# Optimization experiments

Measured on AMD Instinct MI355X. Metric: run time of the kernel, lower is better.

The kernel has to match this reference:

```python
import jax, jax.numpy as jnp
import numpy as np

N_NODES = 131072
N_EDGES = 2097152
F_IN = 128
G_NODES = 256  # nodes per graph (equal-size graphs -> ptr = arange(0, N+1, 256))


def _linear(x, W, b):
    return x @ W + b


def _gin_conv(x, src, dst, W1, b1, W2, b2):
    # GINConv with eps=0: MLP(x + sum_{j->i} x_j)
    agg = jax.ops.segment_sum(x[src], dst, num_segments=x.shape[0])
    h = jax.nn.relu(_linear(x + agg, W1, b1))
    return _linear(h, W2, b2)


def _init(key, fan_in, fan_out):
    kw, kb = jax.random.split(key)
    s = 1.0 / np.sqrt(fan_in)
    W = jax.random.uniform(kw, (fan_in, fan_out), jnp.float32, -s, s)
    b = jax.random.uniform(kb, (fan_out,), jnp.float32, -s, s)
    return W, b


def setup_inputs() -> dict:
    key = jax.random.key(0)
    ks = jax.random.split(key, 14)
    x = jax.random.normal(ks[0], (N_NODES, F_IN), jnp.float32)
    edge_index = jax.random.randint(ks[1], (2, N_EDGES), 0, N_NODES, jnp.int64)
    W1a, b1a = _init(ks[2], F_IN, 128)
    W2a, b2a = _init(ks[3], 128, 128)
    W1b, b1b = _init(ks[4], 128, 128)
    W2b, b2b = _init(ks[5], 128, 128)
    Ws1, bs1 = _init(ks[6], 128, 32)
    Ws2, bs2 = _init(ks[7], 32, 32)
    Ws3, bs3 = _init(ks[8], 32, 32)
    Wm1, bm1 = _init(ks[9], 32 * 32, 32)
    Wm2, bm2 = _init(ks[10], 32, 32)
    Wm3, bm3 = _init(ks[11], 32, 2)
    return dict(x=x, edge_index=edge_index,
                W1a=W1a, b1a=b1a, W2a=W2a, b2a=b2a,
                W1b=W1b, b1b=b1b, W2b=W2b, b2b=b2b,
                Ws1=Ws1, bs1=bs1, Ws2=Ws2, bs2=bs2, Ws3=Ws3, bs3=bs3,
                Wm1=Wm1, bm1=bm1, Wm2=Wm2, bm2=bm2, Wm3=Wm3, bm3=bm3,
                nodes_per_graph=G_NODES)


def reference(x, edge_index, W1a, b1a, W2a, b2a, W1b, b1b, W2b, b2b,
              Ws1, bs1, Ws2, bs2, Ws3, bs3,
              Wm1, bm1, Wm2, bm2, Wm3, bm3, nodes_per_graph):
    src, dst = edge_index[0], edge_index[1]
    # two GINConv layers, each followed by outer ReLU (as in forward)
    h = jax.nn.relu(_gin_conv(x, src, dst, W1a, b1a, W2a, b2a))
    h = jax.nn.relu(_gin_conv(h, src, dst, W1b, b1b, W2b, b2b))
    # dropout is identity in eval mode; F.normalize(dim=1) row-wise L2
    hn = h / jnp.maximum(jnp.linalg.norm(h, axis=1, keepdims=True), 1e-12)
    s = jax.nn.relu(_linear(hn, Ws1, bs1))
    s = jax.nn.relu(_linear(s, Ws2, bs2))
    s = jax.nn.relu(_linear(s, Ws3, bs3))  # [N, 32]
    G = x.shape[0] // nodes_per_graph
    sg = s.reshape(G, nodes_per_graph, 32)
    # per-graph second-order pooling: graph.T @ graph, flattened
    HH = jnp.einsum('gnf,gne->gfe', sg, sg).reshape(G, 32 * 32)  # [G, 1024]
    o = jax.nn.relu(_linear(HH, Wm1, bm1))
    o = jax.nn.relu(_linear(o, Wm2, bm2))
    out = jax.nn.relu(_linear(o, Wm3, bm3))  # [G, 2]; output dropout identity in eval
    return (HH, out)
```

## Files before the change

kernel.cpp:

```cpp
#include <hip/hip_runtime.h>
#include <hip/hip_bf16.h>


#define NN 131072
#define NE 2097152
#define NG 512
#define NB 1024
#define ECAP 2560
#define CCAP 3328
#define ECH 8192

typedef unsigned short u16;
typedef unsigned int u32;
typedef __attribute__((ext_vector_type(8))) short short8;
typedef __attribute__((ext_vector_type(4))) float f32x4;

__device__ __forceinline__ float bf2f(u16 u) {
    union { u32 i; float f; } x; x.i = ((u32)u) << 16; return x.f;
}
__device__ __forceinline__ u16 f2bf(float f) {
    union { u32 i; float f; } x; x.f = f;
    u32 r = x.i + 0x7fffu + ((x.i >> 16) & 1u);
    return (u16)(r >> 16);
}

__global__ __launch_bounds__(256) void cast_x(const float* __restrict__ xf,
                                              u16* __restrict__ xb) {
    int i = blockIdx.x * 256 + threadIdx.x;
    const float4* src = (const float4*)xf;
    float4 a = src[2 * i], b = src[2 * i + 1];
    uint4 o;
    o.x = (u32)f2bf(a.x) | ((u32)f2bf(a.y) << 16);
    o.y = (u32)f2bf(a.z) | ((u32)f2bf(a.w) << 16);
    o.z = (u32)f2bf(b.x) | ((u32)f2bf(b.y) << 16);
    o.w = (u32)f2bf(b.z) | ((u32)f2bf(b.w) << 16);
    ((uint4*)xb)[i] = o;
}

__global__ __launch_bounds__(128) void zero_tail(u16* __restrict__ X0,
                                                 u16* __restrict__ H1) {
    int t = threadIdx.x;
    u32* a = (u32*)(X0 + (size_t)NN * 128);
    u32* b = (u32*)(H1 + (size_t)NN * 128);
    if (t < 64) a[t] = 0; else b[t - 64] = 0;
}

__global__ __launch_bounds__(256) void init_cursor(int* __restrict__ cursor) {
    int b = blockIdx.x * 256 + threadIdx.x;
    cursor[b] = b * ECAP;
}

__global__ __launch_bounds__(256) void bin_scatter(const int* __restrict__ gsrc,
                                                   const int* __restrict__ gdst,
                                                   int* __restrict__ cursor,
                                                   u32* __restrict__ ebuf) {
    __shared__ int lc[NB];
    __shared__ int rb[NB];
    __shared__ int lb[NB];
    int t = threadIdx.x;
    for (int i = 0; i < 4; ++i) lc[t + i * 256] = 0;
    __syncthreads();
    int base = blockIdx.x * ECH;
    for (int i = 0; i < ECH / 256; ++i) {
        int d = gdst[base + i * 256 + t];
        atomicAdd(&lc[d >> 7], 1);
    }
    __syncthreads();
    for (int i = 0; i < 4; ++i) {
        int b = t + i * 256;
        int c = lc[b];
        rb[b] = c ? atomicAdd(&cursor[b], c) : 0;
        lb[b] = 0;
    }
    __syncthreads();
    for (int i = 0; i < ECH / 256; ++i) {
        int idx = base + i * 256 + t;
        int d = gdst[idx];
        int s = gsrc[idx];
        int b = d >> 7;
        int o = atomicAdd(&lb[b], 1);
        ebuf[rb[b] + o] = ((u32)s << 7) | (u32)(d & 127);
    }
}

__global__ __launch_bounds__(512) void csr_sort(const u32* __restrict__ ebuf,
                                                const int* __restrict__ cursor,
                                                int* __restrict__ csr,
                                                int* __restrict__ start,
                                                int* __restrict__ deg) {
    __shared__ int lcnt[128];
    __shared__ int lstart[128];
    __shared__ int lofs[128];
    int t = threadIdx.x, lane = t & 63, wave = t >> 6;
    int bkt = blockIdx.x;
    int e0 = bkt * ECAP;
    int n = cursor[bkt] - e0;
    if (t < 128) lcnt[t] = 0;
    __syncthreads();
    for (int j = t; j < n; j += 512)
        atomicAdd(&lcnt[ebuf[e0 + j] & 127], 1);
    __syncthreads();
    if (wave == 0) {
        int c0 = lcnt[2 * lane], c1 = lcnt[2 * lane + 1];
        int r0 = (c0 + 7) & ~7, r1 = (c1 + 7) & ~7;
        int s = r0 + r1, e = s;
        for (int o = 1; o < 64; o <<= 1) {
            int u = __shfl_up(e, o, 64);
            if (lane >= o) e += u;
        }
        int excl = e - s;
        lstart[2 * lane] = excl;          lofs[2 * lane] = excl;
        lstart[2 * lane + 1] = excl + r0; lofs[2 * lane + 1] = excl + r0;
    }
    __syncthreads();
    for (int j = t; j < n; j += 512) {
        u32 e = ebuf[e0 + j];
        int node = e & 127;
        int pos = atomicAdd(&lofs[node], 1);
        csr[bkt * CCAP + pos] = (int)(e >> 7);
    }
    __syncthreads();
    if (t < 128) {
        int c = lcnt[t];
        int cp = (c + 7) & ~7;
        int base = bkt * CCAP + lstart[t];
        for (int q = c; q < cp; ++q) csr[base + q] = NN;
        start[bkt * 128 + t] = base;
        deg[bkt * 128 + t] = cp;
    }
}

__global__ __launch_bounds__(256) void transpose_w(const float* a, const float* b,
                                                   const float* c, const float* d, u16* Wt) {
    const float* w = (blockIdx.x == 0) ? a : (blockIdx.x == 1) ? b : (blockIdx.x == 2) ? c : d;
    u16* o = Wt + blockIdx.x * 16384;
    for (int i = 0; i < 64; ++i) {
        int idx = threadIdx.x + i * 256;
        o[(idx & 127) * 128 + (idx >> 7)] = f2bf(w[idx]);
    }
}

__global__ __launch_bounds__(256) void transpose_small(const float* Ws1, const float* Ws2,
                                                       const float* Ws3, u16* Wsm) {
    int t = threadIdx.x;
    for (int i = 0; i < 16; ++i) {
        int idx = t + i * 256;
        int k = idx >> 5, n = idx & 31;
        Wsm[n * 128 + k] = f2bf(Ws1[idx]);
    }
    for (int i = 0; i < 4; ++i) {
        int idx = t + i * 256;
        int k = idx >> 5, n = idx & 31;
        Wsm[4096 + n * 32 + k] = f2bf(Ws2[idx]);
        Wsm[5120 + n * 32 + k] = f2bf(Ws3[idx]);
    }
}

__global__ __launch_bounds__(512, 4) void agg_mlp(const u16* __restrict__ X,
                                                  const int* __restrict__ csr,
                                                  const int* __restrict__ start,
                                                  const int* __restrict__ deg,
                                                  const u16* __restrict__ Wt1,
                                                  const u16* __restrict__ Wt2,
                                                  const float* __restrict__ b1,
                                                  const float* __restrict__ b2,
                                                  u16* __restrict__ C) {
    __shared__ u16 As[128][136];
    __shared__ u16 Ws[128][136];
    int tid = threadIdx.x, lane = tid & 63, wave = tid >> 6;
    int quad = lane >> 4, l16 = lane & 15;
    size_t rowBase = (size_t)blockIdx.x * 128;
    const u32* Xu = (const u32*)X;

#pragma unroll
    for (int i = 0; i < 4; ++i) {
        int c = tid + i * 512;
        int r = c >> 4, co = (c & 15) << 3;
        *(uint4*)&Ws[r][co] = *(const uint4*)(Wt1 + r * 128 + co);
    }

    for (int i = 0; i < 16; ++i) {
        int row = (int)rowBase + wave * 16 + i;
        u32 v = Xu[(row << 6) + lane];
        float a0 = bf2f((u16)v), a1 = bf2f((u16)(v >> 16));
        int st = start[row], de = deg[row];
        const int* ip = csr + st;
        for (int p = 0; p < de; p += 8) {
            int4 i0 = *(const int4*)(ip + p);
            int4 i1 = *(const int4*)(ip + p + 4);
            int s[8] = {i0.x, i0.y, i0.z, i0.w, i1.x, i1.y, i1.z, i1.w};
            u32 w[8];
#pragma unroll
            for (int k = 0; k < 8; ++k) w[k] = Xu[(s[k] << 6) + lane];
#pragma unroll
            for (int k = 0; k < 8; ++k) {
                a0 += bf2f((u16)w[k]);
                a1 += bf2f((u16)(w[k] >> 16));
            }
        }
        *(u32*)&As[wave * 16 + i][2 * lane] = (u32)f2bf(a0) | ((u32)f2bf(a1) << 16);
    }
    __syncthreads();

    uint4 w2r[4];
#pragma unroll
    for (int i = 0; i < 4; ++i) {
        int c = tid + i * 512;
        w2r[i] = *(const uint4*)(Wt2 + (c >> 4) * 128 + ((c & 15) << 3));
    }

    f32x4 acc[8];
#pragma unroll
    for (int t = 0; t < 8; ++t) acc[t] = (f32x4){0.f, 0.f, 0.f, 0.f};
#pragma unroll
    for (int c = 0; c < 4; ++c) {
        short8 a = *(const short8*)&As[wave * 16 + l16][c * 32 + quad * 8];
#pragma unroll
        for (int t = 0; t < 8; ++t) {
            short8 b = *(const short8*)&Ws[t * 16 + l16][c * 32 + quad * 8];
            acc[t] = __builtin_amdgcn_mfma_f32_16x16x32_bf16(a, b, acc[t], 0, 0, 0);
        }
    }
#pragma unroll
    for (int t = 0; t < 8; ++t) {
        int col = t * 16 + l16;
        float bv = b1[col];
#pragma unroll
        for (int r = 0; r < 4; ++r)
            As[wave * 16 + quad * 4 + r][col] = f2bf(fmaxf(acc[t][r] + bv, 0.f));
    }
    __syncthreads();

#pragma unroll
    for (int i = 0; i < 4; ++i) {
        int c = tid + i * 512;
        *(uint4*)&Ws[c >> 4][(c & 15) << 3] = w2r[i];
    }
    __syncthreads();

    f32x4 acc2[8];
#pragma unroll
    for (int t = 0; t < 8; ++t) acc2[t] = (f32x4){0.f, 0.f, 0.f, 0.f};
#pragma unroll
    for (int c = 0; c < 4; ++c) {
        short8 a = *(const short8*)&As[wave * 16 + l16][c * 32 + quad * 8];
#pragma unroll
        for (int t = 0; t < 8; ++t) {
            short8 b = *(const short8*)&Ws[t * 16 + l16][c * 32 + quad * 8];
            acc2[t] = __builtin_amdgcn_mfma_f32_16x16x32_bf16(a, b, acc2[t], 0, 0, 0);
        }
    }
#pragma unroll
    for (int t = 0; t < 8; ++t) {
        int col = t * 16 + l16;
        float bv = b2[col];
#pragma unroll
        for (int r = 0; r < 4; ++r) {
            int row = wave * 16 + quad * 4 + r;
            C[(rowBase + row) * 128 + col] = f2bf(fmaxf(acc2[t][r] + bv, 0.f));
        }
    }
}

__global__ __launch_bounds__(256) void norm_mlp_mfma(const u16* __restrict__ X,
                                                     const u16* __restrict__ Wsm,
                                                     const float* __restrict__ bs1,
                                                     const float* __restrict__ bs2,
                                                     const float* __restrict__ bs3,
                                                     float* __restrict__ S) {
    __shared__ u16 As[64][136];
    __shared__ u16 W1s[32][136];
    __shared__ u16 W23s[2][32][40];
    __shared__ u16 H[64][40];
    int tid = threadIdx.x, lane = tid & 63, wave = tid >> 6;
    int quad = lane >> 4, l16 = lane & 15;
    size_t rowBase = (size_t)blockIdx.x * 64;

#pragma unroll
    for (int i = 0; i < 2; ++i) {
        int c = tid + i * 256;
        int r = c >> 4, co = (c & 15) << 3;
        *(uint4*)&W1s[r][co] = *(const uint4*)(Wsm + r * 128 + co);
    }
    {
        int which = tid >> 7, cc = tid & 127;
        int r = cc >> 2, co = (cc & 3) << 3;
        *(uint4*)&W23s[which][r][co] = *(const uint4*)(Wsm + 4096 + which * 1024 + r * 32 + co);
    }

    const u32* Xu = (const u32*)X;
    for (int i = 0; i < 16; ++i) {
        int row = wave * 16 + i;
        u32 v = Xu[(rowBase + row) * 64 + lane];
        float f0 = bf2f((u16)v), f1 = bf2f((u16)(v >> 16));
        float ss = f0 * f0 + f1 * f1;
        for (int o = 1; o < 64; o <<= 1) ss += __shfl_xor(ss, o, 64);
        float inv = 1.0f / fmaxf(sqrtf(ss), 1e-12f);
        *(u32*)&As[row][2 * lane] = (u32)f2bf(f0 * inv) | ((u32)f2bf(f1 * inv) << 16);
    }
    __syncthreads();

    f32x4 acc[2];
    acc[0] = (f32x4){0.f, 0.f, 0.f, 0.f};
    acc[1] = (f32x4){0.f, 0.f, 0.f, 0.f};
#pragma unroll
    for (int c = 0; c < 4; ++c) {
        short8 a = *(const short8*)&As[wave * 16 + l16][c * 32 + quad * 8];
#pragma unroll
        for (int t = 0; t < 2; ++t) {
            short8 b = *(const short8*)&W1s[t * 16 + l16][c * 32 + quad * 8];
            acc[t] = __builtin_amdgcn_mfma_f32_16x16x32_bf16(a, b, acc[t], 0, 0, 0);
        }
    }
#pragma unroll
    for (int t = 0; t < 2; ++t) {
        int col = t * 16 + l16;
        float bv = bs1[col];
#pragma unroll
        for (int r = 0; r < 4; ++r)
            H[wave * 16 + quad * 4 + r][col] = f2bf(fmaxf(acc[t][r] + bv, 0.f));
    }
    __syncthreads();

    f32x4 acc2[2];
    acc2[0] = (f32x4){0.f, 0.f, 0.f, 0.f};
    acc2[1] = (f32x4){0.f, 0.f, 0.f, 0.f};
    {
        short8 a = *(const short8*)&H[wave * 16 + l16][quad * 8];
#pragma unroll
        for (int t = 0; t < 2; ++t) {
            short8 b = *(const short8*)&W23s[0][t * 16 + l16][quad * 8];
            acc2[t] = __builtin_amdgcn_mfma_f32_16x16x32_bf16(a, b, acc2[t], 0, 0, 0);
        }
    }
    __syncthreads();
#pragma unroll
    for (int t = 0; t < 2; ++t) {
        int col = t * 16 + l16;
        float bv = bs2[col];
#pragma unroll
        for (int r = 0; r < 4; ++r)
            H[wave * 16 + quad * 4 + r][col] = f2bf(fmaxf(acc2[t][r] + bv, 0.f));
    }
    __syncthreads();

    f32x4 acc3[2];
    acc3[0] = (f32x4){0.f, 0.f, 0.f, 0.f};
    acc3[1] = (f32x4){0.f, 0.f, 0.f, 0.f};
    {
        short8 a = *(const short8*)&H[wave * 16 + l16][quad * 8];
#pragma unroll
        for (int t = 0; t < 2; ++t) {
            short8 b = *(const short8*)&W23s[1][t * 16 + l16][quad * 8];
            acc3[t] = __builtin_amdgcn_mfma_f32_16x16x32_bf16(a, b, acc3[t], 0, 0, 0);
        }
    }
#pragma unroll
    for (int t = 0; t < 2; ++t) {
        int col = t * 16 + l16;
        float bv = bs3[col];
#pragma unroll
        for (int r = 0; r < 4; ++r) {
            int row = wave * 16 + quad * 4 + r;
            S[(rowBase + row) * 32 + col] = fmaxf(acc3[t][r] + bv, 0.f);
        }
    }
}

__global__ __launch_bounds__(256) void gram(const float* __restrict__ S,
                                            float* __restrict__ out) {
    __shared__ float Sg[256 * 32];
    int t = threadIdx.x, g = blockIdx.x;
    const float4* src = (const float4*)(S + (size_t)g * 8192);
    float4* dst = (float4*)Sg;
    for (int i = 0; i < 8; ++i) dst[t + i * 256] = src[t + i * 256];
    __syncthreads();

    int f = t >> 3, e0 = (t & 7) << 2;
    float4 a = {0.f, 0.f, 0.f, 0.f};
    for (int n = 0; n < 256; ++n) {
        float sf = Sg[n * 32 + f];
        float4 se = *(const float4*)&Sg[n * 32 + e0];
        a.x += sf * se.x; a.y += sf * se.y; a.z += sf * se.z; a.w += sf * se.w;
    }
    *(float4*)(out + (size_t)g * 1024 + f * 32 + e0) = a;
}

__global__ __launch_bounds__(256) void graph_mlp(const float* __restrict__ HH,
                                                 const float* Wm1, const float* bm1,
                                                 const float* Wm2, const float* bm2,
                                                 const float* Wm3, const float* bm3,
                                                 float* __restrict__ out) {
    __shared__ float hh[1024];
    __shared__ float red[256];
    __shared__ float o1[32];
    __shared__ float o2[32];
    int t = threadIdx.x, g = blockIdx.x;
    ((float4*)hh)[t] = ((const float4*)(HH + (size_t)g * 1024))[t];
    __syncthreads();

    int j = t & 31, part = t >> 5;
    float p = 0.f;
    for (int i = 0; i < 128; ++i) { int k = part * 128 + i; p += hh[k] * Wm1[k * 32 + j]; }
    red[t] = p;
    __syncthreads();
    if (t < 32) {
        float s = 0.f;
        for (int q = 0; q < 8; ++q) s += red[q * 32 + t];
        o1[t] = fmaxf(s + bm1[t], 0.f);
    }
    __syncthreads();
    if (t < 32) {
        float s = 0.f;
        for (int k = 0; k < 32; ++k) s += o1[k] * Wm2[k * 32 + t];
        o2[t] = fmaxf(s + bm2[t], 0.f);
    }
    __syncthreads();
    if (t < 2) {
        float s = 0.f;
        for (int k = 0; k < 32; ++k) s += o2[k] * Wm3[k * 2 + t];
        out[524288 + g * 2 + t] = fmaxf(s + bm3[t], 0.f);
    }
}

extern "C" void kernel_launch(void* const* d_in, const int* in_sizes, int n_in,
                              void* d_out, int out_size, void* d_ws, size_t ws_size,
                              hipStream_t stream) {
    const float* x   = (const float*)d_in[0];
    const int*   ei  = (const int*)d_in[1];
    const float* W1a = (const float*)d_in[2];  const float* b1a = (const float*)d_in[3];
    const float* W2a = (const float*)d_in[4];  const float* b2a = (const float*)d_in[5];
    const float* W1b = (const float*)d_in[6];  const float* b1b = (const float*)d_in[7];
    const float* W2b = (const float*)d_in[8];  const float* b2b = (const float*)d_in[9];
    const float* Ws1 = (const float*)d_in[10]; const float* bs1 = (const float*)d_in[11];
    const float* Ws2 = (const float*)d_in[12]; const float* bs2 = (const float*)d_in[13];
    const float* Ws3 = (const float*)d_in[14]; const float* bs3 = (const float*)d_in[15];
    const float* Wm1 = (const float*)d_in[16]; const float* bm1 = (const float*)d_in[17];
    const float* Wm2 = (const float*)d_in[18]; const float* bm2 = (const float*)d_in[19];
    const float* Wm3 = (const float*)d_in[20]; const float* bm3 = (const float*)d_in[21];
    float* out = (float*)d_out;

    const int* gsrc = ei;
    const int* gdst = ei + NE;

    char* ws = (char*)d_ws;
    size_t off = 0;
    auto alloc = [&](size_t bytes) { size_t r = off; off = (off + bytes + 255) & ~(size_t)255; return r; };
    int*  cursor = (int*)(ws + alloc((size_t)NB * 4));
    u32*  ebuf   = (u32*)(ws + alloc((size_t)NB * ECAP * 4));
    int*  csr    = (int*)(ws + alloc((size_t)NB * CCAP * 4));
    int*  stA    = (int*)(ws + alloc((size_t)NN * 4));
    int*  dgA    = (int*)(ws + alloc((size_t)NN * 4));
    u16*  Wt     = (u16*)(ws + alloc(4 * 16384 * 2));
    u16*  Wsm    = (u16*)(ws + alloc(6144 * 2));
    u16*  X0     = (u16*)(ws + alloc((size_t)(NN + 1) * 128 * 2));
    u16*  H1     = (u16*)(ws + alloc((size_t)(NN + 1) * 128 * 2));
    float* S     = (float*)ebuf;
    (void)ws_size; (void)n_in; (void)in_sizes; (void)out_size;

    init_cursor<<<NB / 256, 256, 0, stream>>>(cursor);
    bin_scatter<<<NE / ECH, 256, 0, stream>>>(gsrc, gdst, cursor, ebuf);
    csr_sort<<<NB, 512, 0, stream>>>(ebuf, cursor, csr, stA, dgA);

    cast_x<<<NN * 128 / (256 * 8), 256, 0, stream>>>(x, X0);
    zero_tail<<<1, 128, 0, stream>>>(X0, H1);
    transpose_w<<<4, 256, 0, stream>>>(W1a, W2a, W1b, W2b, Wt);
    transpose_small<<<1, 256, 0, stream>>>(Ws1, Ws2, Ws3, Wsm);

    agg_mlp<<<NN / 128, 512, 0, stream>>>(X0, csr, stA, dgA,
                                          Wt + 0 * 16384, Wt + 1 * 16384, b1a, b2a, H1);
    agg_mlp<<<NN / 128, 512, 0, stream>>>(H1, csr, stA, dgA,
                                          Wt + 2 * 16384, Wt + 3 * 16384, b1b, b2b, X0);

    norm_mlp_mfma<<<NN / 64, 256, 0, stream>>>(X0, Wsm, bs1, bs2, bs3, S);
    gram<<<NG, 256, 0, stream>>>(S, out);
    graph_mlp<<<NG, 256, 0, stream>>>(out, Wm1, bm1, Wm2, bm2, Wm3, bm3, out);
}
```

Baseline: 505.0 us.

## Drop weight LDS staging, prefetch CSR indices per wave, raise agg_mlp occupancy

Removes the shared-memory weight tile and the block-wide barriers, so the MFMA B operands are read straight from global memory (L2/L1 cached). This halves the kernel's LDS use, and launch bounds are raised to allow more resident blocks. The neighbor gather now loads up to 64 CSR indices per row with one coalesced wave load, prefetching the next row's indices, and broadcasts them with readlane instead of having every lane do int4 loads. The costs are redundant global weight reads per wave and the loss of cross-wave sync, which is safe only because each wave uses just its own As rows.

Result: slower. 575.6 us (+14.0%).

```diff
diff --git a/kernel.cpp b/kernel.cpp
--- a/kernel.cpp
+++ b/kernel.cpp
@@ -156,7 +156,7 @@
     }
 }
 
-__global__ __launch_bounds__(512, 4) void agg_mlp(const u16* __restrict__ X,
+__global__ __launch_bounds__(512, 6) void agg_mlp(const u16* __restrict__ X,
                                                   const int* __restrict__ csr,
                                                   const int* __restrict__ start,
                                                   const int* __restrict__ deg,
@@ -165,48 +165,66 @@
                                                   const float* __restrict__ b1,
                                                   const float* __restrict__ b2,
                                                   u16* __restrict__ C) {
-    __shared__ u16 As[128][136];
-    __shared__ u16 Ws[128][136];
+    __shared__ __align__(16) u16 As[128][136];
     int tid = threadIdx.x, lane = tid & 63, wave = tid >> 6;
     int quad = lane >> 4, l16 = lane & 15;
-    size_t rowBase = (size_t)blockIdx.x * 128;
+    int bkt = blockIdx.x;
+    size_t rowBase = (size_t)bkt * 128;
     const u32* Xu = (const u32*)X;
 
-#pragma unroll
-    for (int i = 0; i < 4; ++i) {
-        int c = tid + i * 512;
-        int r = c >> 4, co = (c & 15) << 3;
-        *(uint4*)&Ws[r][co] = *(const uint4*)(Wt1 + r * 128 + co);
-    }
+    int stv = start[(int)rowBase + wave * 16 + (lane & 15)];
+    int dgv = deg[(int)rowBase + wave * 16 + (lane & 15)];
+
+    int st_n = __builtin_amdgcn_readlane(stv, 0);
+    int de_n = __builtin_amdgcn_readlane(dgv, 0);
+    int idx_cur = csr[st_n + min(lane, max(de_n - 1, 0))];
 
     for (int i = 0; i < 16; ++i) {
+        int st = st_n, de = de_n;
         int row = (int)rowBase + wave * 16 + i;
-        u32 v = Xu[(row << 6) + lane];
+        u32 v = Xu[((size_t)row << 6) + lane];
+        int idx = idx_cur;
+        if (i < 15) {
+            st_n = __builtin_amdgcn_readlane(stv, i + 1);
+            de_n = __builtin_amdgcn_readlane(dgv, i + 1);
+            idx_cur = csr[st_n + min(lane, max(de_n - 1, 0))];
+        }
         float a0 = bf2f((u16)v), a1 = bf2f((u16)(v >> 16));
-        int st = start[row], de = deg[row];
-        const int* ip = csr + st;
-        for (int p = 0; p < de; p += 8) {
-            int4 i0 = *(const int4*)(ip + p);
-            int4 i1 = *(const int4*)(ip + p + 4);
-            int s[8] = {i0.x, i0.y, i0.z, i0.w, i1.x, i1.y, i1.z, i1.w};
+        int de64 = min(de, 64);
+        for (int p = 0; p < de64; p += 8) {
             u32 w[8];
 #pragma unroll
-            for (int k = 0; k < 8; ++k) w[k] = Xu[(s[k] << 6) + lane];
+            for (int k = 0; k < 8; ++k) {
+                int s = __builtin_amdgcn_readlane(idx, p + k);
+                w[k] = Xu[((size_t)s << 6) + lane];
+            }
 #pragma unroll
             for (int k = 0; k < 8; ++k) {
                 a0 += bf2f((u16)w[k]);
                 a1 += bf2f((u16)(w[k] >> 16));
             }
         }
-        *(u32*)&As[wave * 16 + i][2 * lane] = (u32)f2bf(a0) | ((u32)f2bf(a1) << 16);
-    }
-    __syncthreads();
-
-    uint4 w2r[4];
-#pragma unroll
-    for (int i = 0; i < 4; ++i) {
-        int c = tid + i * 512;
-        w2r[i] = *(const uint4*)(Wt2 + (c >> 4) * 128 + ((c & 15) << 3));
+        if (de > 64) {
+            for (int pb = 64; pb < de; pb += 64) {
+                int idx2 = csr[st + pb + min(lane, de - pb - 1)];
+                int n2 = min(de - pb, 64);
+                for (int p = 0; p < n2; p += 8) {
+                    u32 w[8];
+#pragma unroll
+                    for (int k = 0; k < 8; ++k) {
+                        int s = __builtin_amdgcn_readlane(idx2, p + k);
+                        w[k] = Xu[((size_t)s << 6) + lane];
+                    }
+#pragma unroll
+                    for (int k = 0; k < 8; ++k) {
+                        a0 += bf2f((u16)w[k]);
+                        a1 += bf2f((u16)(w[k] >> 16));
+                    }
+                }
+            }
+        }
+        *(u32*)&As[wave * 16 + i][2 * lane] =
+            (u32)f2bf(a0) | ((u32)f2bf(a1) << 16);
     }
 
     f32x4 acc[8];
@@ -217,7 +235,7 @@
         short8 a = *(const short8*)&As[wave * 16 + l16][c * 32 + quad * 8];
 #pragma unroll
         for (int t = 0; t < 8; ++t) {
-            short8 b = *(const short8*)&Ws[t * 16 + l16][c * 32 + quad * 8];
+            short8 b = *(const short8*)(Wt1 + (t * 16 + l16) * 128 + c * 32 + quad * 8);
             acc[t] = __builtin_amdgcn_mfma_f32_16x16x32_bf16(a, b, acc[t], 0, 0, 0);
         }
     }
@@ -229,14 +247,6 @@
         for (int r = 0; r < 4; ++r)
             As[wave * 16 + quad * 4 + r][col] = f2bf(fmaxf(acc[t][r] + bv, 0.f));
     }
-    __syncthreads();
-
-#pragma unroll
-    for (int i = 0; i < 4; ++i) {
-        int c = tid + i * 512;
-        *(uint4*)&Ws[c >> 4][(c & 15) << 3] = w2r[i];
-    }
-    __syncthreads();
 
     f32x4 acc2[8];
 #pragma unroll
@@ -246,7 +256,7 @@
         short8 a = *(const short8*)&As[wave * 16 + l16][c * 32 + quad * 8];
 #pragma unroll
         for (int t = 0; t < 8; ++t) {
-            short8 b = *(const short8*)&Ws[t * 16 + l16][c * 32 + quad * 8];
+            short8 b = *(const short8*)(Wt2 + (t * 16 + l16) * 128 + c * 32 + quad * 8);
             acc2[t] = __builtin_amdgcn_mfma_f32_16x16x32_bf16(a, b, acc2[t], 0, 0, 0);
         }
     }
```
